# Performance work log

Measured on AMD Instinct MI355X. Metric: run time of the kernel, lower is better.

## Reference

```python
import jax, jax.numpy as jnp
import numpy as np

B, S, H = 1, 2048, 4096
NH = 32
NOPE, ROPE, VD = 128, 64, 128
QHD = NOPE + ROPE          # 192
QLR, KVLR = 1536, 512
BASE = 10000.0
EPS = 1e-6
SCALE = QHD ** -0.5


def _rmsnorm(x, w):
    xf = x.astype(jnp.float32)
    var = jnp.mean(xf * xf, axis=-1, keepdims=True)
    return (w * (xf * jax.lax.rsqrt(var + EPS))).astype(x.dtype)


def _rope_tables(seq_len):
    inv_freq = 1.0 / (BASE ** (jnp.arange(0, ROPE, 2, dtype=jnp.float32) / ROPE))
    t = jnp.arange(seq_len, dtype=jnp.float32)
    freqs = jnp.outer(t, inv_freq)                     # [S, ROPE/2]
    emb = jnp.concatenate([freqs, freqs], axis=-1)     # [S, ROPE]
    return jnp.cos(emb), jnp.sin(emb)


def _rotate_half(x):
    d = x.shape[-1] // 2
    return jnp.concatenate([-x[..., d:], x[..., :d]], axis=-1)


def setup_inputs() -> dict:
    key = jax.random.key(0)
    ks = jax.random.split(key, 8)
    w = 0.02
    hidden_states = jax.random.normal(ks[0], (B, S, H), dtype=jnp.float32)
    # additive causal mask, 0 on/below diagonal, -1e9 above
    causal = jnp.tril(jnp.ones((S, S), dtype=bool))
    attention_mask = jnp.where(causal, 0.0, -1e9).astype(jnp.float32)[None, None]
    return {
        "hidden_states": hidden_states,
        "attention_mask": attention_mask,
        "Wqa": jax.random.normal(ks[1], (QLR, H), dtype=jnp.float32) * w,
        "qa_ln_w": jnp.ones((QLR,), dtype=jnp.float32),
        "Wqb": jax.random.normal(ks[2], (NH * QHD, QLR), dtype=jnp.float32) * w,
        "Wkva": jax.random.normal(ks[3], (KVLR + ROPE, H), dtype=jnp.float32) * w,
        "kva_ln_w": jnp.ones((KVLR,), dtype=jnp.float32),
        "Wkvb": jax.random.normal(ks[4], (NH * (NOPE + VD), KVLR), dtype=jnp.float32) * w,
        "Wo": jax.random.normal(ks[5], (H, NH * VD), dtype=jnp.float32) * w,
    }


def reference(hidden_states, attention_mask, Wqa, qa_ln_w, Wqb, Wkva, kva_ln_w, Wkvb, Wo):
    bsz, q_len, _ = hidden_states.shape
    # --- Q path: low-rank down-proj + RMSNorm + up-proj ---
    q = _rmsnorm(hidden_states @ Wqa.T, qa_ln_w) @ Wqb.T          # [B,S,NH*QHD]
    q = q.reshape(bsz, q_len, NH, QHD).transpose(0, 2, 1, 3)      # [B,NH,S,QHD]
    q_nope, q_pe = q[..., :NOPE], q[..., NOPE:]
    # --- KV path: shared low-rank compression + decoupled rope key ---
    ckv = hidden_states @ Wkva.T                                   # [B,S,KVLR+ROPE]
    compressed_kv, k_pe = ckv[..., :KVLR], ckv[..., KVLR:]
    k_pe = k_pe.reshape(bsz, q_len, 1, ROPE).transpose(0, 2, 1, 3)  # [B,1,S,ROPE]
    kv = _rmsnorm(compressed_kv, kva_ln_w) @ Wkvb.T                # [B,S,NH*(NOPE+VD)]
    kv = kv.reshape(bsz, q_len, NH, NOPE + VD).transpose(0, 2, 1, 3)
    k_nope, value_states = kv[..., :NOPE], kv[..., NOPE:]
    # --- RoPE on decoupled dims ---
    cos, sin = _rope_tables(q_len)                                 # [S,ROPE] broadcast over B,NH
    q_pe = q_pe * cos + _rotate_half(q_pe) * sin
    k_pe = k_pe * cos + _rotate_half(k_pe) * sin
    query_states = jnp.concatenate([q_nope, q_pe], axis=-1)        # [B,NH,S,QHD]
    key_states = jnp.concatenate(
        [k_nope, jnp.broadcast_to(k_pe, (bsz, NH, q_len, ROPE))], axis=-1)
    # --- SDPA ---
    attn = jnp.einsum('bhqd,bhkd->bhqk', query_states, key_states) * SCALE
    attn = attn + attention_mask
    attn = jax.nn.softmax(attn.astype(jnp.float32), axis=-1).astype(query_states.dtype)
    out = jnp.einsum('bhqk,bhkd->bhqd', attn, value_states)        # [B,NH,S,VD]
    out = out.transpose(0, 2, 1, 3).reshape(bsz, q_len, NH * VD)
    return out @ Wo.T
```

## Files before the change

### kernel.cpp

```cpp
#include <hip/hip_runtime.h>

typedef __bf16 bf16;
typedef __bf16 bf16x8 __attribute__((ext_vector_type(8)));
typedef __bf16 bf16x4 __attribute__((ext_vector_type(4)));
typedef float  f32x4  __attribute__((ext_vector_type(4)));

#define NH_    32
#define S_     2048
#define H_     4096
#define NOPE_  128
#define ROPE_  64
#define VD_    128
#define QHD_   192
#define QLR_   1536
#define KVLR_  512
#define QKVA_N 2176

#define MFMA16(a, b, c) __builtin_amdgcn_mfma_f32_16x16x32_bf16(a, b, c, 0, 0, 0)

__device__ __forceinline__ void async_lds16(void* lds, const void* g) {
  __builtin_amdgcn_global_load_lds(
      (const __attribute__((address_space(1))) void*)g,
      (__attribute__((address_space(3))) void*)lds,
      16, 0, 0);
}

__global__ __launch_bounds__(256) void f2b_kernel(const float* __restrict__ x,
                                                  bf16* __restrict__ y,
                                                  long long n4) {
  long long i = (long long)blockIdx.x * 256 + threadIdx.x;
  long long stride = (long long)gridDim.x * 256;
  for (; i < n4; i += stride) {
    float4 v = ((const float4*)x)[i];
    bf16x4 o;
    o[0] = (bf16)v.x; o[1] = (bf16)v.y; o[2] = (bf16)v.z; o[3] = (bf16)v.w;
    ((bf16x4*)y)[i] = o;
  }
}

__global__ __launch_bounds__(256) void f2b_pad_kernel(const float* __restrict__ x,
                                                      bf16* __restrict__ y,
                                                      long long rows_src, long long cols4,
                                                      long long n4) {
  long long i = (long long)blockIdx.x * 256 + threadIdx.x;
  if (i >= n4) return;
  long long r = i / cols4;
  bf16x4 o;
  if (r < rows_src) {
    float4 v = ((const float4*)x)[i];
    o[0] = (bf16)v.x; o[1] = (bf16)v.y; o[2] = (bf16)v.z; o[3] = (bf16)v.w;
  } else {
    o[0] = o[1] = o[2] = o[3] = (bf16)0.f;
  }
  ((bf16x4*)y)[i] = o;
}

__global__ __launch_bounds__(256) void rope_tables_kernel(float* __restrict__ ct,
                                                          float* __restrict__ st) {
  int i = blockIdx.x * 256 + threadIdx.x;
  int t = i >> 5, f = i & 31;
  float inv = powf(10000.0f, -(float)f / 32.0f);
  float ang = (float)t * inv;
  ct[i] = cosf(ang);
  st[i] = sinf(ang);
}

__global__ __launch_bounds__(256) void rope_q_kernel(bf16* __restrict__ qb,
                                                     const float* __restrict__ ct,
                                                     const float* __restrict__ st) {
  int i = blockIdx.x * 256 + threadIdx.x;
  int t = i >> 10;
  int rem = i & 1023;
  int h = rem >> 5, j = rem & 31;
  size_t base = (size_t)t * (NH_ * QHD_) + h * QHD_ + NOPE_;
  float a = (float)qb[base + j], b = (float)qb[base + 32 + j];
  float c = ct[t * 32 + j], s = st[t * 32 + j];
  qb[base + j]      = (bf16)(a * c - b * s);
  qb[base + 32 + j] = (bf16)(b * c + a * s);
}

__global__ __launch_bounds__(256) void rope_k_kernel(const float* __restrict__ part,
                                                     const float* __restrict__ ct,
                                                     const float* __restrict__ st,
                                                     bf16* __restrict__ kpe,
                                                     long long pstr) {
  int i = blockIdx.x * 256 + threadIdx.x;
  int t = i >> 5, j = i & 31;
  size_t base = (size_t)t * QKVA_N + 2048;
  float a = part[base + j] + part[base + j + pstr];
  float b = part[base + 32 + j] + part[base + 32 + j + pstr];
  float c = ct[i], s = st[i];
  kpe[t * 64 + j]      = (bf16)(a * c - b * s);
  kpe[t * 64 + 32 + j] = (bf16)(b * c + a * s);
}

template <int NS>
__global__ __launch_bounds__(256) void rmsnorm_kernel(const float* __restrict__ x,
                                                      const float* __restrict__ wt,
                                                      bf16* __restrict__ y,
                                                      int cols, int ldx, long long pstr) {
  const int row = blockIdx.x;
  const float* xr = x + (size_t)row * ldx;
  float ss = 0.f;
  for (int i = threadIdx.x; i < cols; i += 256) {
    float v = xr[i];
    if (NS > 1) v += xr[i + pstr];
    ss += v * v;
  }
  __shared__ float red[4];
  for (int off = 32; off > 0; off >>= 1) ss += __shfl_down(ss, off);
  if ((threadIdx.x & 63) == 0) red[threadIdx.x >> 6] = ss;
  __syncthreads();
  float tot = red[0] + red[1] + red[2] + red[3];
  float rr = 1.0f / sqrtf(tot / (float)cols + 1e-6f);
  bf16* yr = y + (size_t)row * cols;
  for (int i = threadIdx.x; i < cols; i += 256) {
    float v = xr[i];
    if (NS > 1) v += xr[i + pstr];
    yr[i] = (bf16)(wt[i] * v * rr);
  }
}

template <typename OutT, bool VOUT = false, int NSPLIT = 1>
__global__ __launch_bounds__(256) void gemm_bt(const bf16* __restrict__ A,
                                               const bf16* __restrict__ B,
                                               OutT* __restrict__ C,
                                               bf16* __restrict__ vTout,
                                               int M, int N, int K) {
  __shared__ bf16 SM[2 * 128 * 64];
  bf16* As = SM;
  bf16* Bs = SM + 128 * 64;
  const int tid = threadIdx.x;
  const int lane = tid & 63;
  const int w = tid >> 6;
  const int wm = w >> 1, wn = w & 1;

  const int nwg = gridDim.x * gridDim.y;
  const int lin = blockIdx.y * gridDim.x + blockIdx.x;
  const int cpx = nwg >> 3;
  const int swz = (lin & 7) * cpx + (lin >> 3);
  const int bx = swz % gridDim.x, by = swz / gridDim.x;

  const int m0 = by * 128, n0 = bx * 128;
  const int r15 = lane & 15;
  const int kbase = (lane >> 4) * 8;

  const int klen = K / NSPLIT;
  const int koff = (NSPLIT > 1) ? (int)blockIdx.z * klen : 0;
  OutT* Cz = (NSPLIT > 1) ? C + (size_t)blockIdx.z * M * (size_t)N : C;

  f32x4 acc[4][4];
#pragma unroll
  for (int i = 0; i < 4; ++i)
#pragma unroll
    for (int j = 0; j < 4; ++j) acc[i][j] = (f32x4){0.f, 0.f, 0.f, 0.f};

  for (int k0 = koff; k0 < koff + klen; k0 += 64) {
    __syncthreads();
#pragma unroll
    for (int s = 0; s < 4; ++s) {
      int lrow = w * 32 + s * 8 + (lane >> 3);
      int sc = (lane & 7) ^ (lrow & 7);
      const bf16* ga = A + (size_t)(m0 + lrow) * K + k0 + sc * 8;
      const bf16* gb = B + (size_t)(n0 + lrow) * K + k0 + sc * 8;
      async_lds16((char*)As + w * 4096 + s * 1024, ga);
      async_lds16((char*)Bs + w * 4096 + s * 1024, gb);
    }
    __syncthreads();

#pragma unroll
    for (int kk = 0; kk < 2; ++kk) {
      bf16x8 af[4], bfr[4];
#pragma unroll
      for (int i = 0; i < 4; ++i) {
        int ar = wm * 64 + i * 16 + r15;
        int off = ar * 128 + (kk * 32 + kbase) * 2;
        off ^= (ar & 7) << 4;
        af[i] = *(const bf16x8*)((const char*)As + off);
      }
#pragma unroll
      for (int j = 0; j < 4; ++j) {
        int br = wn * 64 + j * 16 + r15;
        int off = br * 128 + (kk * 32 + kbase) * 2;
        off ^= (br & 7) << 4;
        bfr[j] = *(const bf16x8*)((const char*)Bs + off);
      }
#pragma unroll
      for (int i = 0; i < 4; ++i)
#pragma unroll
        for (int j = 0; j < 4; ++j)
          acc[i][j] = MFMA16(af[i], bfr[j], acc[i][j]);
    }
  }

  const int rq = lane >> 4;

  if constexpr (VOUT) {
    if (bx & 1) {
      const int hh = bx >> 1;
      __syncthreads();
      bf16* TB = SM;
#pragma unroll
      for (int i = 0; i < 4; ++i)
#pragma unroll
        for (int j = 0; j < 4; ++j) {
          int cl = wn * 64 + j * 16 + r15;
          int rw0 = wm * 64 + i * 16 + rq * 4;
          bf16x4 hv;
#pragma unroll
          for (int r = 0; r < 4; ++r) hv[r] = (bf16)acc[i][j][r];
          *(bf16x4*)&TB[cl * 128 + (rw0 ^ ((cl & 7) << 3))] = hv;
        }
      __syncthreads();
#pragma unroll
      for (int it = 0; it < 8; ++it) {
        int cid = tid + it * 256;
        int dd = cid >> 4, cc = cid & 15;
        bf16x8 v = *(const bf16x8*)&TB[dd * 128 + ((cc ^ (dd & 7)) * 8)];
        *(bf16x8*)(vTout + ((size_t)hh * 128 + dd) * (size_t)M + m0 + cc * 8) = v;
      }
      return;
    }
  }

#pragma unroll
  for (int i = 0; i < 4; ++i)
#pragma unroll
    for (int j = 0; j < 4; ++j)
#pragma unroll
      for (int r = 0; r < 4; ++r) {
        int row = m0 + wm * 64 + i * 16 + rq * 4 + r;
        int col = n0 + wn * 64 + j * 16 + r15;
        Cz[(size_t)row * N + col] = (OutT)acc[i][j][r];
      }
}

__global__ __launch_bounds__(256) void attn_fwd(const bf16* __restrict__ q,
                                                const bf16* __restrict__ kv,
                                                const bf16* __restrict__ vT,
                                                const bf16* __restrict__ kpe,
                                                bf16* __restrict__ out) {
  __shared__ bf16 KN[64][136];
  __shared__ bf16 KP[64][72];
  __shared__ bf16 VS[128 * 64];
  __shared__ bf16 PS[4][16][72];

  const int h = blockIdx.x;
  const int qt = (gridDim.y - 1) - blockIdx.y;
  const int q0 = qt * 64;
  const int tid = threadIdx.x;
  const int lane = tid & 63;
  const int w = tid >> 6;
  const int r15 = lane & 15;
  const int g = lane >> 4;
  const int kbase = g * 8;

  const float SCALE = 0.07216878364870322f;
  const float CS = SCALE * 1.4426950408889634f;
  const float RTH = 8.0f / SCALE;

  bf16x8 qf[6];
  {
    const size_t qrow = q0 + w * 16 + r15;
    const bf16* qp = q + qrow * (NH_ * QHD_) + h * QHD_;
#pragma unroll
    for (int c = 0; c < 6; ++c) qf[c] = *(const bf16x8*)(qp + c * 32 + kbase);
  }

  f32x4 o[9];
#pragma unroll
  for (int d = 0; d < 9; ++d) o[d] = (f32x4){0.f, 0.f, 0.f, 0.f};
  float m[4] = {-1e30f, -1e30f, -1e30f, -1e30f};
  bf16x8 vone;
#pragma unroll
  for (int j = 0; j < 8; ++j) vone[j] = (bf16)1.f;

  const int pr_r = tid >> 4, pr_c = tid & 15;
  const int kp_r = tid >> 2, kp_c = tid & 3;
  const int vd = w * 32 + (lane >> 3);
  const int vc = lane & 7;
  const int vp = vc ^ (vd & 7);
  bf16x8 pKN[4], pV[4], pKP[2];
  auto load_tile = [&](int k0) {
#pragma unroll
    for (int it = 0; it < 4; ++it) {
      pKN[it] = *(const bf16x8*)(kv + (size_t)(k0 + pr_r + it * 16) * (NH_ * 256) + h * 256 + pr_c * 8);
      pV[it]  = *(const bf16x8*)(vT + ((size_t)h * 128 + vd + it * 8) * (size_t)S_ + k0 + vc * 8);
    }
    pKP[0] = *(const bf16x8*)(kpe + (size_t)(k0 + kp_r) * 64 + kp_c * 16);
    pKP[1] = *(const bf16x8*)(kpe + (size_t)(k0 + kp_r) * 64 + kp_c * 16 + 8);
  };

  load_tile(0);

  for (int kt = 0; kt <= qt; ++kt) {
    const int k0 = kt * 64;
    __syncthreads();
#pragma unroll
    for (int it = 0; it < 4; ++it) {
      *(bf16x8*)&KN[pr_r + it * 16][pr_c * 8] = pKN[it];
      *(bf16x8*)((char*)VS + (vd + it * 8) * 128 + vp * 16) = pV[it];
    }
    *(bf16x8*)&KP[kp_r][kp_c * 16] = pKP[0];
    *(bf16x8*)&KP[kp_r][kp_c * 16 + 8] = pKP[1];
    __syncthreads();

    if (kt < qt) load_tile(k0 + 64);

    f32x4 s[4];
    __builtin_amdgcn_s_setprio(1);
#pragma unroll
    for (int ct = 0; ct < 4; ++ct) {
      f32x4 a = (f32x4){0.f, 0.f, 0.f, 0.f};
#pragma unroll
      for (int c = 0; c < 4; ++c) {
        bf16x8 b = *(const bf16x8*)&KN[ct * 16 + r15][c * 32 + kbase];
        a = MFMA16(qf[c], b, a);
      }
#pragma unroll
      for (int c = 0; c < 2; ++c) {
        bf16x8 b = *(const bf16x8*)&KP[ct * 16 + r15][c * 32 + kbase];
        a = MFMA16(qf[4 + c], b, a);
      }
      s[ct] = a;
    }
    __builtin_amdgcn_s_setprio(0);

    const int qrow0 = q0 + w * 16 + g * 4;
    if (kt == qt) {
#pragma unroll
      for (int ct = 0; ct < 4; ++ct)
#pragma unroll
        for (int r = 0; r < 4; ++r)
          if ((k0 + ct * 16 + r15) > (qrow0 + r)) s[ct][r] = -1e30f;
    }

    float lm[4];
#pragma unroll
    for (int r = 0; r < 4; ++r)
      lm[r] = fmaxf(fmaxf(s[0][r], s[1][r]), fmaxf(s[2][r], s[3][r]));
    bool over = (lm[0] > m[0] + RTH) || (lm[1] > m[1] + RTH) ||
                (lm[2] > m[2] + RTH) || (lm[3] > m[3] + RTH);
    if (__any(over)) {
#pragma unroll
      for (int r = 0; r < 4; ++r) {
        float v = lm[r];
        v = fmaxf(v, __shfl_xor(v, 1));
        v = fmaxf(v, __shfl_xor(v, 2));
        v = fmaxf(v, __shfl_xor(v, 4));
        v = fmaxf(v, __shfl_xor(v, 8));
        float mn = fmaxf(m[r], v);
        float sc = exp2f((m[r] - mn) * CS);
        m[r] = mn;
#pragma unroll
        for (int d = 0; d < 9; ++d) o[d][r] *= sc;
      }
    }
#pragma unroll
    for (int ct = 0; ct < 4; ++ct)
#pragma unroll
      for (int r = 0; r < 4; ++r)
        PS[w][g * 4 + r][ct * 16 + r15] = (bf16)exp2f((s[ct][r] - m[r]) * CS);

    __builtin_amdgcn_s_setprio(1);
#pragma unroll
    for (int kk = 0; kk < 2; ++kk) {
      bf16x8 pa = *(const bf16x8*)&PS[w][r15][kk * 32 + kbase];
      const int kcx = (kk * 4 + g) ^ (r15 & 7);
      o[8] = MFMA16(pa, vone, o[8]);
#pragma unroll
      for (int dt = 0; dt < 8; ++dt) {
        int d = dt * 16 + r15;
        bf16x8 vb = *(const bf16x8*)((const char*)VS + d * 128 + kcx * 16);
        o[dt] = MFMA16(pa, vb, o[dt]);
      }
    }
    __builtin_amdgcn_s_setprio(0);
  }

  float invl[4];
#pragma unroll
  for (int r = 0; r < 4; ++r) invl[r] = 1.0f / o[8][r];
#pragma unroll
  for (int dt = 0; dt < 8; ++dt)
#pragma unroll
    for (int r = 0; r < 4; ++r) {
      int row = q0 + w * 16 + g * 4 + r;
      out[(size_t)row * (NH_ * VD_) + h * VD_ + dt * 16 + r15] = (bf16)(o[dt][r] * invl[r]);
    }
}

extern "C" void kernel_launch(void* const* d_in, const int* in_sizes, int n_in,
                              void* d_out, int out_size, void* d_ws, size_t ws_size,
                              hipStream_t stream) {
  (void)in_sizes; (void)n_in; (void)out_size; (void)ws_size;
  const float* hs     = (const float*)d_in[0];
  const float* Wqa    = (const float*)d_in[2];
  const float* qa_ln  = (const float*)d_in[3];
  const float* Wqb    = (const float*)d_in[4];
  const float* Wkva   = (const float*)d_in[5];
  const float* kva_ln = (const float*)d_in[6];
  const float* Wkvb   = (const float*)d_in[7];
  const float* Wo     = (const float*)d_in[8];
  float* outp = (float*)d_out;

  char* W = (char*)d_ws;
  size_t off = 0;
  auto nxt = [&](size_t b) { size_t o = off; off += (b + 255) & ~(size_t)255; return o; };
  bf16*  hidden_bf = (bf16*)(W + nxt((size_t)S_ * H_ * 2));
  bf16*  qkva_w    = (bf16*)(W + nxt((size_t)QKVA_N * H_ * 2));
  bf16*  Wqb_bf    = (bf16*)(W + nxt((size_t)NH_ * QHD_ * QLR_ * 2));
  bf16*  Wkvb_bf   = (bf16*)(W + nxt((size_t)NH_ * 256 * KVLR_ * 2));
  bf16*  Wo_bf     = (bf16*)(W + nxt((size_t)H_ * NH_ * VD_ * 2));
  bf16*  qa_norm   = (bf16*)(W + nxt((size_t)S_ * QLR_ * 2));
  bf16*  ckv_norm  = (bf16*)(W + nxt((size_t)S_ * KVLR_ * 2));
  bf16*  kpe       = (bf16*)(W + nxt((size_t)S_ * ROPE_ * 2));
  float* cost      = (float*)(W + nxt((size_t)S_ * 32 * 4));
  float* sint      = (float*)(W + nxt((size_t)S_ * 32 * 4));
  size_t Roff = nxt((size_t)S_ * NH_ * QHD_ * 2 + (size_t)S_ * NH_ * 256 * 2 +
                    (size_t)NH_ * VD_ * S_ * 2 + (size_t)S_ * NH_ * VD_ * 2);
  bf16* q_bf     = (bf16*)(W + Roff);
  bf16* kv_bf    = (bf16*)(W + Roff + (size_t)S_ * NH_ * QHD_ * 2);
  bf16* vT       = (bf16*)(W + Roff + (size_t)S_ * NH_ * QHD_ * 2 + (size_t)S_ * NH_ * 256 * 2);
  bf16* attn_out = (bf16*)(W + Roff + (size_t)S_ * NH_ * QHD_ * 2 + (size_t)S_ * NH_ * 256 * 2 +
                           (size_t)NH_ * VD_ * S_ * 2);
  float* part    = (float*)(W + Roff);
  const long long PSTR = (long long)S_ * QKVA_N;

  f2b_kernel<<<8192, 256, 0, stream>>>(hs, hidden_bf, (long long)S_ * H_ / 4);
  f2b_kernel<<<6144, 256, 0, stream>>>(Wqa, qkva_w, (long long)QLR_ * H_ / 4);
  f2b_pad_kernel<<<2560, 256, 0, stream>>>(Wkva, qkva_w + (size_t)QLR_ * H_, 576, H_ / 4,
                                           (long long)640 * H_ / 4);
  f2b_kernel<<<9216, 256, 0, stream>>>(Wqb, Wqb_bf, (long long)NH_ * QHD_ * QLR_ / 4);
  f2b_kernel<<<4096, 256, 0, stream>>>(Wkvb, Wkvb_bf, (long long)NH_ * 256 * KVLR_ / 4);
  f2b_kernel<<<16384, 256, 0, stream>>>(Wo, Wo_bf, (long long)H_ * NH_ * VD_ / 4);
  rope_tables_kernel<<<256, 256, 0, stream>>>(cost, sint);

  gemm_bt<float, false, 2><<<dim3(QKVA_N / 128, S_ / 128, 2), 256, 0, stream>>>(
      hidden_bf, qkva_w, part, nullptr, S_, QKVA_N, H_);

  rmsnorm_kernel<2><<<S_, 256, 0, stream>>>(part, qa_ln, qa_norm, QLR_, QKVA_N, PSTR);
  rmsnorm_kernel<2><<<S_, 256, 0, stream>>>(part + QLR_, kva_ln, ckv_norm, KVLR_, QKVA_N, PSTR);
  rope_k_kernel<<<256, 256, 0, stream>>>(part, cost, sint, kpe, PSTR);

  gemm_bt<bf16><<<dim3(NH_ * QHD_ / 128, S_ / 128), 256, 0, stream>>>(
      qa_norm, Wqb_bf, q_bf, nullptr, S_, NH_ * QHD_, QLR_);
  rope_q_kernel<<<8192, 256, 0, stream>>>(q_bf, cost, sint);

  gemm_bt<bf16, true><<<dim3(NH_ * 256 / 128, S_ / 128), 256, 0, stream>>>(
      ckv_norm, Wkvb_bf, kv_bf, vT, S_, NH_ * 256, KVLR_);

  attn_fwd<<<dim3(NH_, S_ / 64), 256, 0, stream>>>(q_bf, kv_bf, vT, kpe, attn_out);

  gemm_bt<float><<<dim3(H_ / 128, S_ / 128), 256, 0, stream>>>(
      attn_out, Wo_bf, outp, nullptr, S_, H_, H_);
}
```

Baseline: 391.6 us.

## Pair complementary causal query tiles per block to share K/V loads

Each attention block now processes two query tiles, p and 31-p, over a shared K/V stream, so every block does equal causal work and each K/V tile loaded into LDS serves both tiles. The grid is halved accordingly. This removes causal load imbalance and halves K/V global traffic. In exchange, register use per thread doubles (two sets of Q fragments and accumulators), which lowers occupancy, and there are fewer blocks to fill the GPU.

```diff
diff --git a/kernel.cpp b/kernel.cpp
--- a/kernel.cpp
+++ b/kernel.cpp
@@ -246,8 +246,9 @@
   __shared__ bf16 PS[4][16][72];
 
   const int h = blockIdx.x;
-  const int qt = (gridDim.y - 1) - blockIdx.y;
-  const int q0 = qt * 64;
+  const int p = blockIdx.y;
+  const int qtA = p, qtB = 31 - p;
+  const int qA0 = qtA * 64, qB0 = qtB * 64;
   const int tid = threadIdx.x;
   const int lane = tid & 63;
   const int w = tid >> 6;
@@ -259,18 +260,26 @@
   const float CS = SCALE * 1.4426950408889634f;
   const float RTH = 8.0f / SCALE;
 
-  bf16x8 qf[6];
+  bf16x8 qfA[6], qfB[6];
   {
-    const size_t qrow = q0 + w * 16 + r15;
-    const bf16* qp = q + qrow * (NH_ * QHD_) + h * QHD_;
-#pragma unroll
-    for (int c = 0; c < 6; ++c) qf[c] = *(const bf16x8*)(qp + c * 32 + kbase);
-  }
-
-  f32x4 o[9];
-#pragma unroll
-  for (int d = 0; d < 9; ++d) o[d] = (f32x4){0.f, 0.f, 0.f, 0.f};
-  float m[4] = {-1e30f, -1e30f, -1e30f, -1e30f};
+    const bf16* qpA = q + (size_t)(qA0 + w * 16 + r15) * (NH_ * QHD_) + h * QHD_;
+    const bf16* qpB = q + (size_t)(qB0 + w * 16 + r15) * (NH_ * QHD_) + h * QHD_;
+#pragma unroll
+    for (int c = 0; c < 6; ++c) {
+      qfA[c] = *(const bf16x8*)(qpA + c * 32 + kbase);
+      qfB[c] = *(const bf16x8*)(qpB + c * 32 + kbase);
+    }
+  }
+
+  f32x4 oA[9], oB[9];
+#pragma unroll
+  for (int d = 0; d < 9; ++d) {
+    oA[d] = (f32x4){0.f, 0.f, 0.f, 0.f};
+    oB[d] = (f32x4){0.f, 0.f, 0.f, 0.f};
+  }
+  float mA[4], mB[4];
+#pragma unroll
+  for (int r = 0; r < 4; ++r) { mA[r] = mB[r] = -1e30f; }
   bf16x8 vone;
 #pragma unroll
   for (int j = 0; j < 8; ++j) vone[j] = (bf16)1.f;
@@ -293,20 +302,7 @@
 
   load_tile(0);
 
-  for (int kt = 0; kt <= qt; ++kt) {
-    const int k0 = kt * 64;
-    __syncthreads();
-#pragma unroll
-    for (int it = 0; it < 4; ++it) {
-      *(bf16x8*)&KN[pr_r + it * 16][pr_c * 8] = pKN[it];
-      *(bf16x8*)((char*)VS + (vd + it * 8) * 128 + vp * 16) = pV[it];
-    }
-    *(bf16x8*)&KP[kp_r][kp_c * 16] = pKP[0];
-    *(bf16x8*)&KP[kp_r][kp_c * 16 + 8] = pKP[1];
-    __syncthreads();
-
-    if (kt < qt) load_tile(k0 + 64);
-
+  auto process = [&](const bf16x8* qf, f32x4* o, float* m, int q0t, bool diag, int k0) {
     f32x4 s[4];
     __builtin_amdgcn_s_setprio(1);
 #pragma unroll
@@ -326,8 +322,8 @@
     }
     __builtin_amdgcn_s_setprio(0);
 
-    const int qrow0 = q0 + w * 16 + g * 4;
-    if (kt == qt) {
+    const int qrow0 = q0t + w * 16 + g * 4;
+    if (diag) {
 #pragma unroll
       for (int ct = 0; ct < 4; ++ct)
 #pragma unroll
@@ -376,17 +372,40 @@
       }
     }
     __builtin_amdgcn_s_setprio(0);
-  }
-
-  float invl[4];
-#pragma unroll
-  for (int r = 0; r < 4; ++r) invl[r] = 1.0f / o[8][r];
+  };
+
+  for (int kt = 0; kt <= qtB; ++kt) {
+    const int k0 = kt * 64;
+    __syncthreads();
+#pragma unroll
+    for (int it = 0; it < 4; ++it) {
+      *(bf16x8*)&KN[pr_r + it * 16][pr_c * 8] = pKN[it];
+      *(bf16x8*)((char*)VS + (vd + it * 8) * 128 + vp * 16) = pV[it];
+    }
+    *(bf16x8*)&KP[kp_r][kp_c * 16] = pKP[0];
+    *(bf16x8*)&KP[kp_r][kp_c * 16 + 8] = pKP[1];
+    __syncthreads();
+
+    if (kt < qtB) load_tile(k0 + 64);
+
+    if (kt <= qtA) process(qfA, oA, mA, qA0, kt == qtA, k0);
+    process(qfB, oB, mB, qB0, kt == qtB, k0);
+  }
+
+  float invA[4], invB[4];
+#pragma unroll
+  for (int r = 0; r < 4; ++r) {
+    invA[r] = 1.0f / oA[8][r];
+    invB[r] = 1.0f / oB[8][r];
+  }
 #pragma unroll
   for (int dt = 0; dt < 8; ++dt)
 #pragma unroll
     for (int r = 0; r < 4; ++r) {
-      int row = q0 + w * 16 + g * 4 + r;
-      out[(size_t)row * (NH_ * VD_) + h * VD_ + dt * 16 + r15] = (bf16)(o[dt][r] * invl[r]);
+      int rowA = qA0 + w * 16 + g * 4 + r;
+      int rowB = qB0 + w * 16 + g * 4 + r;
+      out[(size_t)rowA * (NH_ * VD_) + h * VD_ + dt * 16 + r15] = (bf16)(oA[dt][r] * invA[r]);
+      out[(size_t)rowB * (NH_ * VD_) + h * VD_ + dt * 16 + r15] = (bf16)(oB[dt][r] * invB[r]);
     }
 }
 
@@ -450,7 +469,7 @@
   gemm_bt<bf16, true><<<dim3(NH_ * 256 / 128, S_ / 128), 256, 0, stream>>>(
       ckv_norm, Wkvb_bf, kv_bf, vT, S_, NH_ * 256, KVLR_);
 
-  attn_fwd<<<dim3(NH_, S_ / 64), 256, 0, stream>>>(q_bf, kv_bf, vT, kpe, attn_out);
+  attn_fwd<<<dim3(NH_, 16), 256, 0, stream>>>(q_bf, kv_bf, vT, kpe, attn_out);
 
   gemm_bt<float><<<dim3(H_ / 128, S_ / 128), 256, 0, stream>>>(
       attn_out, Wo_bf, outp, nullptr, S_, H_, H_);
```

Result: slower. 431.7 us (median of 2 runs) (+10.3%).
